# Kernel tuning notes

Hardware: AMD Instinct MI355X
Metric: run time of the kernel (lower is better)

## Reference

```python
import jax, jax.numpy as jnp
import numpy as np

N, E, NFEAT, NHID, NCLASS = 50000, 800000, 256, 128, 16
NTRAIN, NTEST, K = 5000, 5000, 20


def setup_inputs() -> dict:
    key = jax.random.key(0)
    ks = jax.random.split(key, 10)
    features = jax.random.normal(ks[0], (N, NFEAT), dtype=jnp.float32)
    edge_index = jax.random.randint(ks[1], (2, E), 0, N, dtype=jnp.int64)
    edge_weight = jax.random.uniform(ks[2], (E,), dtype=jnp.float32)
    labels = jax.random.randint(ks[3], (N,), 0, NCLASS)
    onehot_labels = jax.nn.one_hot(labels, NCLASS, dtype=jnp.float32)
    idx_train = jax.random.randint(ks[4], (NTRAIN,), 0, N, dtype=jnp.int64)
    idx_test = jax.random.randint(ks[5], (NTEST,), 0, N, dtype=jnp.int64)
    # GCN parameters (2-layer: nfeat->nhid->nhid), glorot-ish init
    W1 = jax.random.normal(ks[6], (NFEAT, NHID), dtype=jnp.float32) / np.sqrt(NFEAT)
    b1 = jnp.zeros((NHID,), dtype=jnp.float32)
    W2 = jax.random.normal(ks[7], (NHID, NHID), dtype=jnp.float32) / np.sqrt(NHID)
    b2 = jnp.zeros((NHID,), dtype=jnp.float32)
    return {"features": features, "edge_weight": edge_weight,
            "onehot_labels": onehot_labels, "W1": W1, "b1": b1,
            "W2": W2, "b2": b2, "edge_index": edge_index,
            "idx_train": idx_train, "idx_test": idx_test}


def _propagate(h, edge_index, edge_weight, n_nodes):
    # out[dst] += w * h[src]  (weighted message passing)
    src, dst = edge_index[0], edge_index[1]
    return jax.ops.segment_sum(h[src] * edge_weight[:, None], dst,
                               num_segments=n_nodes)


def reference(features, edge_weight, onehot_labels, W1, b1, W2, b2,
              edge_index, idx_train, idx_test):
    n_nodes = features.shape[0]
    # 2-layer GCN: transform then propagate (efficient order)
    h = _propagate(features @ W1, edge_index, edge_weight, n_nodes) + b1
    h = jax.nn.relu(h)
    emb = _propagate(h @ W2, edge_index, edge_weight, n_nodes) + b2

    # KNN scoring: [n_test, n_train] similarity matrix
    score = emb[idx_test] @ emb[idx_train].T
    # keep top-K largest per row (original masks the n_train-K smallest with -inf)
    vals, idx = jax.lax.top_k(score, K)
    rows = jnp.arange(score.shape[0])[:, None]
    masked = jnp.full_like(score, -jnp.inf).at[rows, idx].set(vals)
    weights = jax.nn.softmax(masked, axis=1)
    preds = weights @ onehot_labels[idx_train]
    return preds
```

## Files before the change

### kernel.cpp

```cpp
#include <hip/hip_runtime.h>
#include <math.h>
#include <limits.h>

#define NNODE 50000
#define NEDGE 800000
#define NFEAT 256
#define NHID  128
#define NTEST 5000
#define NTRAIN 5000
#define NCLS  16
#define TOPK  20
#define CB    640
#define NCT   8
#define RB    32
#define NTPAD (NCT * CB)
#define NTGT  (NTPAD + NTEST)
#define CCAP  512
#define GB1   ((NNODE + 63) / 64)
#define FB1   ((NEDGE + 255) / 256)

typedef __attribute__((ext_vector_type(8))) short short8v;
typedef __attribute__((ext_vector_type(4))) short short4v;
typedef __attribute__((ext_vector_type(4))) float f32x4;

__device__ inline int swz(int r, int c) {
  int cc = c + 4 * r;
  cc = (cc < CB) ? cc : cc - CB;
  return r * CB + cc;
}

__device__ inline void splitbf(float x, unsigned short& h, unsigned short& l) {
  unsigned u = __float_as_uint(x);
  unsigned hb = (u + 0x7fffu + ((u >> 16) & 1u)) >> 16;
  float hf = __uint_as_float(hb << 16);
  float r = x - hf;
  unsigned ur = __float_as_uint(r);
  unsigned lb = (ur + 0x7fffu + ((ur >> 16) & 1u)) >> 16;
  h = (unsigned short)hb; l = (unsigned short)lb;
}

__device__ inline void split8(float4 a0, float4 a1, short8v& h, short8v& l) {
  unsigned short hh, ll;
  splitbf(a0.x, hh, ll); h[0] = (short)hh; l[0] = (short)ll;
  splitbf(a0.y, hh, ll); h[1] = (short)hh; l[1] = (short)ll;
  splitbf(a0.z, hh, ll); h[2] = (short)hh; l[2] = (short)ll;
  splitbf(a0.w, hh, ll); h[3] = (short)hh; l[3] = (short)ll;
  splitbf(a1.x, hh, ll); h[4] = (short)hh; l[4] = (short)ll;
  splitbf(a1.y, hh, ll); h[5] = (short)hh; l[5] = (short)ll;
  splitbf(a1.z, hh, ll); h[6] = (short)hh; l[6] = (short)ll;
  splitbf(a1.w, hh, ll); h[7] = (short)hh; l[7] = (short)ll;
}

__global__ __launch_bounds__(256)
void prep_hist(const float* __restrict__ W1, unsigned short* __restrict__ WT1hi,
               unsigned short* __restrict__ WT1lo,
               const float* __restrict__ W2, unsigned short* __restrict__ WT2hi,
               unsigned short* __restrict__ WT2lo,
               const float* __restrict__ onehot, const int* __restrict__ itr,
               float* __restrict__ lab, int* __restrict__ ccnt,
               const int* __restrict__ edst, int* __restrict__ cursor) {
  int gid = blockIdx.x * 256 + threadIdx.x;
  if (gid < NFEAT * 128) {
    int n = gid / NFEAT, k = gid - n * NFEAT;
    unsigned short h, l;
    splitbf(W1[(size_t)k * 128 + n], h, l);
    WT1hi[gid] = h; WT1lo[gid] = l;
  } else if (gid < NFEAT * 128 + NHID * 128) {
    int i = gid - NFEAT * 128;
    int n = i / NHID, k = i - n * NHID;
    unsigned short h, l;
    splitbf(W2[(size_t)k * 128 + n], h, l);
    WT2hi[i] = h; WT2lo[i] = l;
  } else if (gid < NFEAT * 128 + NHID * 128 + NTRAIN * NCLS) {
    int i = gid - NFEAT * 128 - NHID * 128;
    int j = i >> 4, c = i & 15;
    lab[i] = onehot[(size_t)itr[j] * NCLS + c];
  } else if (gid < NFEAT * 128 + NHID * 128 + NTRAIN * NCLS + NTEST) {
    ccnt[gid - NFEAT * 128 - NHID * 128 - NTRAIN * NCLS] = 0;
  } else if (gid < NFEAT * 128 + NHID * 128 + NTRAIN * NCLS + NTEST + NEDGE) {
    int e = gid - NFEAT * 128 - NHID * 128 - NTRAIN * NCLS - NTEST;
    atomicAdd(&cursor[edst[e]], 1);
  }
}

#define SCHUNK 49
__global__ __launch_bounds__(1024)
void scan_cnt(int* __restrict__ cnt) {
  __shared__ int part[1024];
  const int t = threadIdx.x;
  const int base = t * SCHUNK;
  int s = 0;
  {
    int idx = base;
#pragma unroll
    for (int i = 0; i < 12; ++i, idx += 4) {
      if (idx + 3 < NNODE) {
        int4 v = *reinterpret_cast<const int4*>(&cnt[idx]);
        s += v.x + v.y + v.z + v.w;
      } else {
        for (int j = 0; j < 4; ++j) if (idx + j < NNODE) s += cnt[idx + j];
      }
    }
    if (idx < NNODE) s += cnt[idx];
  }
  part[t] = s;
  __syncthreads();
  for (int off = 1; off < 1024; off <<= 1) {
    int v = (t >= off) ? part[t - off] : 0;
    __syncthreads();
    part[t] += v;
    __syncthreads();
  }
  int run = part[t] - s;
  {
    int idx = base;
#pragma unroll
    for (int i = 0; i < 12; ++i, idx += 4) {
      if (idx + 3 < NNODE) {
        int4 v = *reinterpret_cast<const int4*>(&cnt[idx]);
        int4 o;
        o.x = run; run += v.x; o.y = run; run += v.y;
        o.z = run; run += v.z; o.w = run; run += v.w;
        *reinterpret_cast<int4*>(&cnt[idx]) = o;
      } else {
        for (int j = 0; j < 4; ++j)
          if (idx + j < NNODE) { int c = cnt[idx + j]; cnt[idx + j] = run; run += c; }
      }
    }
    if (idx < NNODE) { int c = cnt[idx]; cnt[idx] = run; run += c; }
  }
}

__global__ __launch_bounds__(256)
void gemm1_fill(const float* __restrict__ A, const unsigned short* __restrict__ WThi,
                const unsigned short* __restrict__ WTlo, float* __restrict__ C,
                const int* __restrict__ esrc, const int* __restrict__ edst,
                const float* __restrict__ ew, int* __restrict__ cursor,
                int2* __restrict__ packed) {
  const int tid = threadIdx.x;
  if (blockIdx.x >= GB1) {
    int e = (blockIdx.x - GB1) * 256 + tid;
    if (e < NEDGE) {
      int d = edst[e];
      int p = atomicAdd(&cursor[d], 1);
      packed[p] = make_int2(esrc[e], __float_as_int(ew[e]));
    }
    return;
  }
  const int w = tid >> 6, lane = tid & 63;
  const int m0 = blockIdx.x * 64 + w * 16;
  int arow = m0 + (lane & 15); if (arow > NNODE - 1) arow = NNODE - 1;
  const int koff = (lane >> 4) * 8;

  float4 av0[8], av1[8];
#pragma unroll
  for (int ks = 0; ks < 8; ++ks) {
    const float* ap = &A[(size_t)arow * NFEAT + ks * 32 + koff];
    av0[ks] = *reinterpret_cast<const float4*>(ap);
    av1[ks] = *reinterpret_cast<const float4*>(ap + 4);
  }

  f32x4 acc[8];
#pragma unroll
  for (int t = 0; t < 8; ++t) acc[t] = {0.f, 0.f, 0.f, 0.f};

#pragma unroll
  for (int ks = 0; ks < 8; ++ks) {
    short8v ah, al;
    split8(av0[ks], av1[ks], ah, al);
#pragma unroll
    for (int t = 0; t < 8; ++t) {
      size_t bo = (size_t)(t * 16 + (lane & 15)) * NFEAT + ks * 32 + koff;
      short8v bh = *reinterpret_cast<const short8v*>(&WThi[bo]);
      short8v bl = *reinterpret_cast<const short8v*>(&WTlo[bo]);
      acc[t] = __builtin_amdgcn_mfma_f32_16x16x32_bf16(ah, bh, acc[t], 0, 0, 0);
      acc[t] = __builtin_amdgcn_mfma_f32_16x16x32_bf16(ah, bl, acc[t], 0, 0, 0);
      acc[t] = __builtin_amdgcn_mfma_f32_16x16x32_bf16(al, bh, acc[t], 0, 0, 0);
    }
  }
  const int crow0 = m0 + (lane >> 4) * 4;
#pragma unroll
  for (int j = 0; j < 4; ++j) {
    int row = crow0 + j;
    if (row < NNODE) {
#pragma unroll
      for (int t = 0; t < 8; ++t)
        C[(size_t)row * 128 + t * 16 + (lane & 15)] = acc[t][j];
    }
  }
}

__global__ __launch_bounds__(256)
void gather_nodes(const float* __restrict__ X, float* __restrict__ out,
                  const int* __restrict__ endoff, const int2* __restrict__ packed,
                  const float* __restrict__ bias) {
  const int tid = threadIdx.x;
  const int node = blockIdx.x * 4 + (tid >> 6);
  const int lane = tid & 63;
  const int half = lane >> 5, c4 = lane & 31;
  const int beg = node ? endoff[node - 1] : 0;
  const int end = endoff[node];
  const float4* X4 = reinterpret_cast<const float4*>(X);
  float4 a0 = {0.f,0.f,0.f,0.f}, a1 = {0.f,0.f,0.f,0.f};
  float4 a2 = {0.f,0.f,0.f,0.f}, a3 = {0.f,0.f,0.f,0.f};
  int e = beg + half;
  for (; e + 6 < end; e += 8) {
    int2 p0 = packed[e],     p1 = packed[e + 2];
    int2 p2 = packed[e + 4], p3 = packed[e + 6];
    float4 x0 = X4[(size_t)p0.x * 32 + c4];
    float4 x1 = X4[(size_t)p1.x * 32 + c4];
    float4 x2 = X4[(size_t)p2.x * 32 + c4];
    float4 x3 = X4[(size_t)p3.x * 32 + c4];
    float w0 = __int_as_float(p0.y), w1 = __int_as_float(p1.y);
    float w2 = __int_as_float(p2.y), w3 = __int_as_float(p3.y);
    a0.x += w0*x0.x; a0.y += w0*x0.y; a0.z += w0*x0.z; a0.w += w0*x0.w;
    a1.x += w1*x1.x; a1.y += w1*x1.y; a1.z += w1*x1.z; a1.w += w1*x1.w;
    a2.x += w2*x2.x; a2.y += w2*x2.y; a2.z += w2*x2.z; a2.w += w2*x2.w;
    a3.x += w3*x3.x; a3.y += w3*x3.y; a3.z += w3*x3.z; a3.w += w3*x3.w;
  }
  for (; e < end; e += 2) {
    int2 p = packed[e];
    float4 x = X4[(size_t)p.x * 32 + c4];
    float w = __int_as_float(p.y);
    a0.x += w*x.x; a0.y += w*x.y; a0.z += w*x.z; a0.w += w*x.w;
  }
  a0.x += a1.x + a2.x + a3.x; a0.y += a1.y + a2.y + a3.y;
  a0.z += a1.z + a2.z + a3.z; a0.w += a1.w + a2.w + a3.w;
  a0.x += __shfl_xor(a0.x, 32); a0.y += __shfl_xor(a0.y, 32);
  a0.z += __shfl_xor(a0.z, 32); a0.w += __shfl_xor(a0.w, 32);
  if (half == 0) {
    float4 b = reinterpret_cast<const float4*>(bias)[c4];
    a0.x += b.x; a0.y += b.y; a0.z += b.z; a0.w += b.w;
    reinterpret_cast<float4*>(out)[(size_t)node * 32 + c4] = a0;
  }
}

__global__ __launch_bounds__(256)
void gather_targets2(const float* __restrict__ H, const int* __restrict__ endoff,
                     const int2* __restrict__ packed,
                     const int* __restrict__ itr, const int* __restrict__ ite,
                     float* __restrict__ g) {
  const int tid = threadIdx.x;
  const int tgt = blockIdx.x * 4 + (tid >> 6);
  const int lane = tid & 63;
  const int half = lane >> 5, c4 = lane & 31;
  const bool isQ = tgt >= NTPAD;
  const int j = isQ ? tgt - NTPAD : tgt;
  int node = -1;
  if (isQ) { if (j < NTEST) node = ite[j]; }
  else if (j < NTRAIN) node = itr[j];

  float4 a0 = {0.f, 0.f, 0.f, 0.f};
  if (node >= 0) {
    const int beg = node ? endoff[node - 1] : 0;
    const int end = endoff[node];
    const float4* X4 = reinterpret_cast<const float4*>(H);
    float4 a1 = {0.f,0.f,0.f,0.f}, a2 = {0.f,0.f,0.f,0.f}, a3 = {0.f,0.f,0.f,0.f};
    int e = beg + half;
    for (; e + 6 < end; e += 8) {
      int2 p0 = packed[e],     p1 = packed[e + 2];
      int2 p2 = packed[e + 4], p3 = packed[e + 6];
      float4 x0 = X4[(size_t)p0.x * 32 + c4];
      float4 x1 = X4[(size_t)p1.x * 32 + c4];
      float4 x2 = X4[(size_t)p2.x * 32 + c4];
      float4 x3 = X4[(size_t)p3.x * 32 + c4];
      float w0 = __int_as_float(p0.y), w1 = __int_as_float(p1.y);
      float w2 = __int_as_float(p2.y), w3 = __int_as_float(p3.y);
      a0.x += w0*fmaxf(x0.x,0.f); a0.y += w0*fmaxf(x0.y,0.f);
      a0.z += w0*fmaxf(x0.z,0.f); a0.w += w0*fmaxf(x0.w,0.f);
      a1.x += w1*fmaxf(x1.x,0.f); a1.y += w1*fmaxf(x1.y,0.f);
      a1.z += w1*fmaxf(x1.z,0.f); a1.w += w1*fmaxf(x1.w,0.f);
      a2.x += w2*fmaxf(x2.x,0.f); a2.y += w2*fmaxf(x2.y,0.f);
      a2.z += w2*fmaxf(x2.z,0.f); a2.w += w2*fmaxf(x2.w,0.f);
      a3.x += w3*fmaxf(x3.x,0.f); a3.y += w3*fmaxf(x3.y,0.f);
      a3.z += w3*fmaxf(x3.z,0.f); a3.w += w3*fmaxf(x3.w,0.f);
    }
    for (; e < end; e += 2) {
      int2 p = packed[e];
      float4 x = X4[(size_t)p.x * 32 + c4];
      float w = __int_as_float(p.y);
      a0.x += w*fmaxf(x.x,0.f); a0.y += w*fmaxf(x.y,0.f);
      a0.z += w*fmaxf(x.z,0.f); a0.w += w*fmaxf(x.w,0.f);
    }
    a0.x += a1.x + a2.x + a3.x; a0.y += a1.y + a2.y + a3.y;
    a0.z += a1.z + a2.z + a3.z; a0.w += a1.w + a2.w + a3.w;
    a0.x += __shfl_xor(a0.x, 32); a0.y += __shfl_xor(a0.y, 32);
    a0.z += __shfl_xor(a0.z, 32); a0.w += __shfl_xor(a0.w, 32);
  }
  if (half == 0 && tgt < NTGT)
    reinterpret_cast<float4*>(g)[(size_t)tgt * 32 + c4] = a0;
}

__global__ __launch_bounds__(256)
void mini_gemm(const float* __restrict__ A, const unsigned short* __restrict__ WThi,
               const unsigned short* __restrict__ WTlo, const float* __restrict__ b2,
               unsigned short* __restrict__ Thi, unsigned short* __restrict__ Tlo,
               unsigned short* __restrict__ Qhi, unsigned short* __restrict__ Qlo) {
  const int tid = threadIdx.x;
  const int w = tid >> 6, lane = tid & 63;
  const int m0 = blockIdx.x * 64 + w * 16;
  int arow = m0 + (lane & 15); if (arow > NTGT - 1) arow = NTGT - 1;
  const int koff = (lane >> 4) * 8;

  float4 av0[4], av1[4];
#pragma unroll
  for (int ks = 0; ks < 4; ++ks) {
    const float* ap = &A[(size_t)arow * NHID + ks * 32 + koff];
    av0[ks] = *reinterpret_cast<const float4*>(ap);
    av1[ks] = *reinterpret_cast<const float4*>(ap + 4);
  }

  f32x4 acc[8];
#pragma unroll
  for (int t = 0; t < 8; ++t) acc[t] = {0.f, 0.f, 0.f, 0.f};

#pragma unroll
  for (int ks = 0; ks < 4; ++ks) {
    short8v ah, al;
    split8(av0[ks], av1[ks], ah, al);
#pragma unroll
    for (int t = 0; t < 8; ++t) {
      size_t bo = (size_t)(t * 16 + (lane & 15)) * NHID + ks * 32 + koff;
      short8v bh = *reinterpret_cast<const short8v*>(&WThi[bo]);
      short8v bl = *reinterpret_cast<const short8v*>(&WTlo[bo]);
      acc[t] = __builtin_amdgcn_mfma_f32_16x16x32_bf16(ah, bh, acc[t], 0, 0, 0);
      acc[t] = __builtin_amdgcn_mfma_f32_16x16x32_bf16(ah, bl, acc[t], 0, 0, 0);
      acc[t] = __builtin_amdgcn_mfma_f32_16x16x32_bf16(al, bh, acc[t], 0, 0, 0);
    }
  }
  const int crow0 = m0 + (lane >> 4) * 4;
#pragma unroll
  for (int j = 0; j < 4; ++j) {
    int row = crow0 + j;
    if (row < NTGT) {
#pragma unroll
      for (int t = 0; t < 8; ++t) {
        int col = t * 16 + (lane & 15);
        float val = acc[t][j] + b2[col];
        unsigned short h, l;
        splitbf(val, h, l);
        if (row < NTPAD) {
          Thi[(size_t)row * 128 + col] = h;
          Tlo[(size_t)row * 128 + col] = l;
        } else {
          Qhi[(size_t)(row - NTPAD) * 128 + col] = h;
          Qlo[(size_t)(row - NTPAD) * 128 + col] = l;
        }
      }
    }
  }
}

__global__ __launch_bounds__(512)
void score_mfma(const unsigned short* __restrict__ Qhi, const unsigned short* __restrict__ Qlo,
                const unsigned short* __restrict__ Thi, const unsigned short* __restrict__ Tlo,
                int* __restrict__ ccnt, float* __restrict__ candv, int* __restrict__ candi) {
  __shared__ float s[2 * 16 * CB];
  const int tid = threadIdx.x;
  const int w = tid >> 6, lane = tid & 63;
  const int r0 = (blockIdx.x >> 3) * RB;
  const int j0 = (blockIdx.x & 7) * CB;

  int arow0 = r0 + (lane & 15);      if (arow0 > NTEST - 1) arow0 = NTEST - 1;
  int arow1 = r0 + 16 + (lane & 15); if (arow1 > NTEST - 1) arow1 = NTEST - 1;
  const int koff = (lane >> 4) * 8;
  short8v ah0[4], al0[4], ah1[4], al1[4];
#pragma unroll
  for (int ks = 0; ks < 4; ++ks) {
    ah0[ks] = *reinterpret_cast<const short8v*>(&Qhi[(size_t)arow0 * 128 + ks * 32 + koff]);
    al0[ks] = *reinterpret_cast<const short8v*>(&Qlo[(size_t)arow0 * 128 + ks * 32 + koff]);
    ah1[ks] = *reinterpret_cast<const short8v*>(&Qhi[(size_t)arow1 * 128 + ks * 32 + koff]);
    al1[ks] = *reinterpret_cast<const short8v*>(&Qlo[(size_t)arow1 * 128 + ks * 32 + koff]);
  }

#pragma unroll
  for (int t = 0; t < 5; ++t) {
    int colbase = w * 80 + t * 16;
    int col = j0 + colbase + (lane & 15);
    const unsigned short* bh = &Thi[(size_t)col * 128 + koff];
    const unsigned short* bl = &Tlo[(size_t)col * 128 + koff];
    f32x4 a0 = {0.f, 0.f, 0.f, 0.f};
    f32x4 a1 = {0.f, 0.f, 0.f, 0.f};
#pragma unroll
    for (int ks = 0; ks < 4; ++ks) {
      short8v bhv = *reinterpret_cast<const short8v*>(&bh[ks * 32]);
      short8v blv = *reinterpret_cast<const short8v*>(&bl[ks * 32]);
      a0 = __builtin_amdgcn_mfma_f32_16x16x32_bf16(ah0[ks], bhv, a0, 0, 0, 0);
      a1 = __builtin_amdgcn_mfma_f32_16x16x32_bf16(ah1[ks], bhv, a1, 0, 0, 0);
      a0 = __builtin_amdgcn_mfma_f32_16x16x32_bf16(ah0[ks], blv, a0, 0, 0, 0);
      a1 = __builtin_amdgcn_mfma_f32_16x16x32_bf16(ah1[ks], blv, a1, 0, 0, 0);
      a0 = __builtin_amdgcn_mfma_f32_16x16x32_bf16(al0[ks], bhv, a0, 0, 0, 0);
      a1 = __builtin_amdgcn_mfma_f32_16x16x32_bf16(al1[ks], bhv, a1, 0, 0, 0);
    }
    int sc = colbase + (lane & 15);
    int sr = (lane >> 4) * 4;
#pragma unroll
    for (int r = 0; r < 4; ++r) s[swz(sr + r, sc)] = a0[r];
#pragma unroll
    for (int r = 0; r < 4; ++r) s[16 * CB + swz(sr + r, sc)] = a1[r];
  }
  __syncthreads();

  const unsigned long long ltm = ((unsigned long long)1 << lane) - 1;

#pragma unroll
  for (int g = 0; g < 2; ++g) {
    const float* sg = s + g * 16 * CB;
#pragma unroll
    for (int r = 0; r < 2; ++r) {
      const int m = w * 2 + r;
      const int row = r0 + g * 16 + m;
      if (row >= NTEST) continue;
      float v[10];
#pragma unroll
      for (int k = 0; k < 10; ++k) {
        int c = lane + 64 * k;
        v[k] = (j0 + c < NTRAIN) ? sg[swz(m, c)] : -INFINITY;
      }
      float t0 = fmaxf(v[0], v[1]), t1 = fmaxf(v[2], v[3]);
      float t2 = fmaxf(v[4], v[5]), t3 = fmaxf(v[6], v[7]);
      float sv = fmaxf(fmaxf(fmaxf(t0, t1), fmaxf(t2, t3)), fmaxf(v[8], v[9]));
#pragma unroll
      for (int k = 2; k <= 64; k <<= 1) {
#pragma unroll
        for (int j = k >> 1; j > 0; j >>= 1) {
          float ov = __shfl_xor(sv, j);
          bool keepMax = ((lane & j) == 0) == ((lane & k) == 0 || k == 64);
          sv = keepMax ? fmaxf(sv, ov) : fminf(sv, ov);
        }
      }
      float T = __shfl(sv, 19);

      int myo[10];
      int tot = 0;
#pragma unroll
      for (int k = 0; k < 10; ++k) {
        unsigned long long mk = __ballot(v[k] >= T);
        myo[k] = tot + (int)__popcll(mk & ltm);
        tot += (int)__popcll(mk);
      }
      if (tot <= 64) {
        int base = 0;
        if (lane == 0) base = atomicAdd(&ccnt[row], tot);
        base = __shfl(base, 0);
        float* cv = candv + (size_t)row * CCAP + base;
        int*   ci = candi + (size_t)row * CCAP + base;
#pragma unroll
        for (int k = 0; k < 10; ++k) {
          if (v[k] >= T) { cv[myo[k]] = v[k]; ci[myo[k]] = j0 + lane + 64 * k; }
        }
      } else {
        float selv = 0.f; int seli = 0;
#pragma unroll
        for (int it = 0; it < TOPK; ++it) {
          float bv = v[0]; int bk = 0;
#pragma unroll
          for (int k = 1; k < 10; ++k)
            if (v[k] > bv) { bv = v[k]; bk = k; }
          int bj = lane + 64 * bk;
#pragma unroll
          for (int off = 1; off < 64; off <<= 1) {
            float ov = __shfl_xor(bv, off);
            int   oj = __shfl_xor(bj, off);
            if (ov > bv || (ov == bv && oj < bj)) { bv = ov; bj = oj; }
          }
          if (lane == it) { selv = bv; seli = j0 + bj; }
          int ck = bj >> 6;
          if ((bj & 63) == lane) {
#pragma unroll
            for (int k = 0; k < 10; ++k)
              if (k == ck) v[k] = -INFINITY;
          }
        }
        int base = 0;
        if (lane == 0) base = atomicAdd(&ccnt[row], TOPK);
        base = __shfl(base, 0);
        if (lane < TOPK) {
          candv[(size_t)row * CCAP + base + lane] = selv;
          candi[(size_t)row * CCAP + base + lane] = seli;
        }
      }
    }
  }
}

__device__ inline void sort64_vi(float& v, int& idx, int lane) {
#pragma unroll
  for (int k = 2; k <= 64; k <<= 1) {
#pragma unroll
    for (int j = k >> 1; j > 0; j >>= 1) {
      float ov = __shfl_xor(v, j);
      int   oi = __shfl_xor(idx, j);
      bool first = (v > ov) || (v == ov && idx < oi);
      bool keepMine = (((lane & j) == 0) == ((lane & k) == 0 || k == 64)) ? first : !first;
      if (!keepMine) { v = ov; idx = oi; }
    }
  }
}

__global__ __launch_bounds__(256)
void merge_topk(const float* __restrict__ candv, const int* __restrict__ candi,
                const int* __restrict__ ccnt, const float* __restrict__ lab,
                float* __restrict__ out) {
  const int tid = threadIdx.x;
  const int wv = tid >> 6, lane = tid & 63;
  const int row = blockIdx.x * 4 + wv;
  const size_t base = (size_t)row * CCAP;
  const int C = ccnt[row];

  float v = -INFINITY; int idx = INT_MAX;
  int take = C < 64 ? C : 64;
  if (lane < take) { v = candv[base + lane]; idx = candi[base + lane]; }
  sort64_vi(v, idx, lane);
  int consumed = take;
  while (consumed < C) {
    int n = C - consumed; if (n > 44) n = 44;
    if (lane >= TOPK) {
      int p = lane - TOPK;
      if (p < n) { v = candv[base + consumed + p]; idx = candi[base + consumed + p]; }
      else       { v = -INFINITY; idx = INT_MAX; }
    }
    sort64_vi(v, idx, lane);
    consumed += n;
  }
  float mx = __shfl(v, 0);
  float wgt = (lane < TOPK) ? expf(v - mx) : 0.f;
  float sum = wgt;
#pragma unroll
  for (int off = 1; off < 64; off <<= 1) sum += __shfl_xor(sum, off);

  float acc = 0.f;
#pragma unroll
  for (int i = 0; i < TOPK; ++i) {
    float wi = __shfl(wgt, i);
    int   ji = __shfl(idx, i);
    if (lane < NCLS) acc += wi * lab[(size_t)ji * NCLS + lane];
  }
  if (lane < NCLS) out[(size_t)row * NCLS + lane] = acc / sum;
}

extern "C" void kernel_launch(void* const* d_in, const int* in_sizes, int n_in,
                              void* d_out, int out_size, void* d_ws, size_t ws_size,
                              hipStream_t stream) {
  const float* feat   = (const float*)d_in[0];
  const float* ew     = (const float*)d_in[1];
  const float* onehot = (const float*)d_in[2];
  const float* W1     = (const float*)d_in[3];
  const float* b1     = (const float*)d_in[4];
  const float* W2     = (const float*)d_in[5];
  const float* b2     = (const float*)d_in[6];
  const int*   ei     = (const int*)d_in[7];
  const int*   itr    = (const int*)d_in[8];
  const int*   ite    = (const int*)d_in[9];
  float* out = (float*)d_out;
  float* ws  = (float*)d_ws;

  float* bufA   = ws;
  float* bufH   = bufA + (size_t)NNODE * NHID;
  int*   cursor = (int*)(bufH + (size_t)NNODE * NHID);
  int2*  packed = (int2*)(cursor + ((NNODE + 15) & ~15));
  unsigned short* WT1hi = (unsigned short*)(packed + NEDGE);
  unsigned short* WT1lo = WT1hi + 128 * NFEAT;
  unsigned short* WT2hi = WT1lo + 128 * NFEAT;
  unsigned short* WT2lo = WT2hi + 128 * NHID;
  float* lab  = (float*)(WT2lo + 128 * NHID);
  int*   ccnt = (int*)(lab + (size_t)NTRAIN * NCLS);
  unsigned short* Thi = (unsigned short*)bufA;
  unsigned short* Tlo = Thi + (size_t)NTPAD * NHID;
  unsigned short* Qhi = Tlo + (size_t)NTPAD * NHID;
  unsigned short* Qlo = Qhi + (size_t)NTEST * NHID;
  float* g    = (float*)(Qlo + (size_t)NTEST * NHID);
  float* candv = bufH;
  int*   candi = (int*)(bufH + (size_t)NTEST * CCAP);

  const int* esrc = ei;
  const int* edst = ei + NEDGE;

  hipMemsetAsync(cursor, 0, NNODE * sizeof(int), stream);
  int ptot = NFEAT * 128 + NHID * 128 + NTRAIN * NCLS + NTEST + NEDGE;
  prep_hist<<<(ptot + 255) / 256, 256, 0, stream>>>(
      W1, WT1hi, WT1lo, W2, WT2hi, WT2lo, onehot, itr, lab, ccnt, edst, cursor);
  scan_cnt<<<1, 1024, 0, stream>>>(cursor);
  gemm1_fill<<<GB1 + FB1, 256, 0, stream>>>(
      feat, WT1hi, WT1lo, bufA, esrc, edst, ew, cursor, packed);

  gather_nodes<<<NNODE / 4, 256, 0, stream>>>(bufA, bufH, cursor, packed, b1);
  gather_targets2<<<(NTGT + 3) / 4, 256, 0, stream>>>(bufH, cursor, packed, itr, ite, g);
  mini_gemm<<<(NTGT + 63) / 64, 256, 0, stream>>>(
      g, WT2hi, WT2lo, b2, Thi, Tlo, Qhi, Qlo);

  score_mfma<<<((NTEST + RB - 1) / RB) * NCT, 512, 0, stream>>>(
      Qhi, Qlo, Thi, Tlo, ccnt, candv, candi);
  merge_topk<<<NTEST / 4, 256, 0, stream>>>(candv, candi, ccnt, lab, out);
}
```

Measured before the change: 324.9 us.

## Stage gemm1 A tiles through LDS with direct global-to-LDS loads

gemm1_fill now loads each 64x32 A slice into shared memory with global_load_lds (16-byte direct copies) instead of preloading all 8 K-slices into registers, then reads the MFMA fragments back from LDS, with two barriers per K step. mini_gemm interleaves its A loads with the MFMA loop instead of preloading everything. The aim is to cut register pressure and raise occupancy, and to get more coalesced row-wise global reads. The cost is per-iteration barriers and loss of load/compute overlap, since there is no double buffering.

```diff
diff --git a/kernel.cpp b/kernel.cpp
--- a/kernel.cpp
+++ b/kernel.cpp
@@ -22,6 +22,10 @@
 typedef __attribute__((ext_vector_type(8))) short short8v;
 typedef __attribute__((ext_vector_type(4))) short short4v;
 typedef __attribute__((ext_vector_type(4))) float f32x4;
+
+#define GLOAD_LDS16(g, l) __builtin_amdgcn_global_load_lds( \
+    (const __attribute__((address_space(1))) void*)(g),     \
+    (__attribute__((address_space(3))) void*)(l), 16, 0, 0)
 
 __device__ inline int swz(int r, int c) {
   int cc = c + 4 * r;
@@ -147,27 +151,25 @@
     }
     return;
   }
+  __shared__ float tile[2048];
   const int w = tid >> 6, lane = tid & 63;
-  const int m0 = blockIdx.x * 64 + w * 16;
-  int arow = m0 + (lane & 15); if (arow > NNODE - 1) arow = NNODE - 1;
-  const int koff = (lane >> 4) * 8;
-
-  float4 av0[8], av1[8];
-#pragma unroll
+  const int bm = blockIdx.x * 64;
+  int grow = bm + lane; if (grow > NNODE - 1) grow = NNODE - 1;
+  const int s0f = (((lane >> 4) * 2) * 64 + w * 16 + (lane & 15)) * 4;
+
+  f32x4 acc[8];
+#pragma unroll
+  for (int t = 0; t < 8; ++t) acc[t] = {0.f, 0.f, 0.f, 0.f};
+
   for (int ks = 0; ks < 8; ++ks) {
-    const float* ap = &A[(size_t)arow * NFEAT + ks * 32 + koff];
-    av0[ks] = *reinterpret_cast<const float4*>(ap);
-    av1[ks] = *reinterpret_cast<const float4*>(ap + 4);
-  }
-
-  f32x4 acc[8];
-#pragma unroll
-  for (int t = 0; t < 8; ++t) acc[t] = {0.f, 0.f, 0.f, 0.f};
-
-#pragma unroll
-  for (int ks = 0; ks < 8; ++ks) {
+    GLOAD_LDS16(&A[(size_t)grow * NFEAT + ks * 32 + w * 4],       &tile[w * 256]);
+    GLOAD_LDS16(&A[(size_t)grow * NFEAT + ks * 32 + (4 + w) * 4], &tile[(4 + w) * 256]);
+    __syncthreads();
+    float4 a0 = *reinterpret_cast<const float4*>(&tile[s0f]);
+    float4 a1 = *reinterpret_cast<const float4*>(&tile[s0f + 256]);
     short8v ah, al;
-    split8(av0[ks], av1[ks], ah, al);
+    split8(a0, a1, ah, al);
+    const int koff = (lane >> 4) * 8;
 #pragma unroll
     for (int t = 0; t < 8; ++t) {
       size_t bo = (size_t)(t * 16 + (lane & 15)) * NFEAT + ks * 32 + koff;
@@ -177,8 +179,9 @@
       acc[t] = __builtin_amdgcn_mfma_f32_16x16x32_bf16(ah, bl, acc[t], 0, 0, 0);
       acc[t] = __builtin_amdgcn_mfma_f32_16x16x32_bf16(al, bh, acc[t], 0, 0, 0);
     }
-  }
-  const int crow0 = m0 + (lane >> 4) * 4;
+    __syncthreads();
+  }
+  const int crow0 = bm + w * 16 + (lane >> 4) * 4;
 #pragma unroll
   for (int j = 0; j < 4; ++j) {
     int row = crow0 + j;
@@ -302,22 +305,17 @@
   int arow = m0 + (lane & 15); if (arow > NTGT - 1) arow = NTGT - 1;
   const int koff = (lane >> 4) * 8;
 
-  float4 av0[4], av1[4];
+  f32x4 acc[8];
+#pragma unroll
+  for (int t = 0; t < 8; ++t) acc[t] = {0.f, 0.f, 0.f, 0.f};
+
 #pragma unroll
   for (int ks = 0; ks < 4; ++ks) {
     const float* ap = &A[(size_t)arow * NHID + ks * 32 + koff];
-    av0[ks] = *reinterpret_cast<const float4*>(ap);
-    av1[ks] = *reinterpret_cast<const float4*>(ap + 4);
-  }
-
-  f32x4 acc[8];
-#pragma unroll
-  for (int t = 0; t < 8; ++t) acc[t] = {0.f, 0.f, 0.f, 0.f};
-
-#pragma unroll
-  for (int ks = 0; ks < 4; ++ks) {
+    float4 a0 = *reinterpret_cast<const float4*>(ap);
+    float4 a1 = *reinterpret_cast<const float4*>(ap + 4);
     short8v ah, al;
-    split8(av0[ks], av1[ks], ah, al);
+    split8(a0, a1, ah, al);
 #pragma unroll
     for (int t = 0; t < 8; ++t) {
       size_t bo = (size_t)(t * 16 + (lane & 15)) * NHID + ks * 32 + koff;
```

After: 357.9 us. +10.2%, slower.

## Shard edge fill by destination range and interleave A loads with MFMA

Applied to the files above, without the earlier changes.

The edge-fill part of the fused gemm1 kernel now launches eight times as many blocks. Each edge chunk is read by eight blocks, and each block writes only the edges whose destination falls in its own node range, so concurrent atomics and scattered writes stay inside a smaller region. It also drops the up-front preload of all A rows in the gemm1 and mini_gemm kernels and loads each k-slice right before its MFMAs, which lowers register pressure. In exchange, the edge arrays are read eight times, the extra per-edge division adds work, and latency hiding on the A loads may get worse.

```diff
diff --git a/kernel.cpp b/kernel.cpp
--- a/kernel.cpp
+++ b/kernel.cpp
@@ -17,7 +17,8 @@
 #define NTGT  (NTPAD + NTEST)
 #define CCAP  512
 #define GB1   ((NNODE + 63) / 64)
-#define FB1   ((NEDGE + 255) / 256)
+#define FB8   (8 * ((NEDGE + 255) / 256))
+#define DSHARD 6250
 
 typedef __attribute__((ext_vector_type(8))) short short8v;
 typedef __attribute__((ext_vector_type(4))) short short4v;
@@ -139,11 +140,16 @@
                 int2* __restrict__ packed) {
   const int tid = threadIdx.x;
   if (blockIdx.x >= GB1) {
-    int e = (blockIdx.x - GB1) * 256 + tid;
+    int i = blockIdx.x - GB1;
+    int chunk = i >> 3;
+    int range = blockIdx.x & 7;
+    int e = chunk * 256 + tid;
     if (e < NEDGE) {
       int d = edst[e];
-      int p = atomicAdd(&cursor[d], 1);
-      packed[p] = make_int2(esrc[e], __float_as_int(ew[e]));
+      if (d / DSHARD == range) {
+        int p = atomicAdd(&cursor[d], 1);
+        packed[p] = make_int2(esrc[e], __float_as_int(ew[e]));
+      }
     }
     return;
   }
@@ -152,22 +158,17 @@
   int arow = m0 + (lane & 15); if (arow > NNODE - 1) arow = NNODE - 1;
   const int koff = (lane >> 4) * 8;
 
-  float4 av0[8], av1[8];
+  f32x4 acc[8];
+#pragma unroll
+  for (int t = 0; t < 8; ++t) acc[t] = {0.f, 0.f, 0.f, 0.f};
+
 #pragma unroll
   for (int ks = 0; ks < 8; ++ks) {
     const float* ap = &A[(size_t)arow * NFEAT + ks * 32 + koff];
-    av0[ks] = *reinterpret_cast<const float4*>(ap);
-    av1[ks] = *reinterpret_cast<const float4*>(ap + 4);
-  }
-
-  f32x4 acc[8];
-#pragma unroll
-  for (int t = 0; t < 8; ++t) acc[t] = {0.f, 0.f, 0.f, 0.f};
-
-#pragma unroll
-  for (int ks = 0; ks < 8; ++ks) {
+    float4 a0 = *reinterpret_cast<const float4*>(ap);
+    float4 a1 = *reinterpret_cast<const float4*>(ap + 4);
     short8v ah, al;
-    split8(av0[ks], av1[ks], ah, al);
+    split8(a0, a1, ah, al);
 #pragma unroll
     for (int t = 0; t < 8; ++t) {
       size_t bo = (size_t)(t * 16 + (lane & 15)) * NFEAT + ks * 32 + koff;
@@ -302,22 +303,17 @@
   int arow = m0 + (lane & 15); if (arow > NTGT - 1) arow = NTGT - 1;
   const int koff = (lane >> 4) * 8;
 
-  float4 av0[4], av1[4];
+  f32x4 acc[8];
+#pragma unroll
+  for (int t = 0; t < 8; ++t) acc[t] = {0.f, 0.f, 0.f, 0.f};
+
 #pragma unroll
   for (int ks = 0; ks < 4; ++ks) {
     const float* ap = &A[(size_t)arow * NHID + ks * 32 + koff];
-    av0[ks] = *reinterpret_cast<const float4*>(ap);
-    av1[ks] = *reinterpret_cast<const float4*>(ap + 4);
-  }
-
-  f32x4 acc[8];
-#pragma unroll
-  for (int t = 0; t < 8; ++t) acc[t] = {0.f, 0.f, 0.f, 0.f};
-
-#pragma unroll
-  for (int ks = 0; ks < 4; ++ks) {
+    float4 a0 = *reinterpret_cast<const float4*>(ap);
+    float4 a1 = *reinterpret_cast<const float4*>(ap + 4);
     short8v ah, al;
-    split8(av0[ks], av1[ks], ah, al);
+    split8(a0, a1, ah, al);
 #pragma unroll
     for (int t = 0; t < 8; ++t) {
       size_t bo = (size_t)(t * 16 + (lane & 15)) * NHID + ks * 32 + koff;
@@ -581,7 +577,7 @@
   prep_hist<<<(ptot + 255) / 256, 256, 0, stream>>>(
       W1, WT1hi, WT1lo, W2, WT2hi, WT2lo, onehot, itr, lab, ccnt, edst, cursor);
   scan_cnt<<<1, 1024, 0, stream>>>(cursor);
-  gemm1_fill<<<GB1 + FB1, 256, 0, stream>>>(
+  gemm1_fill<<<GB1 + FB8, 256, 0, stream>>>(
       feat, WT1hi, WT1lo, bufA, esrc, edst, ew, cursor, packed);
 
   gather_nodes<<<NNODE / 4, 256, 0, stream>>>(bufA, bufH, cursor, packed, b1);
```

Result: slower. 341.0 us (+5.0%).
